# Optimization experiments

Measured on AMD Instinct MI355X. Metric: run time of the kernel, lower is better.

Reference implementation:

```python
import jax, jax.numpy as jnp
import numpy as np

N = 50000      # nodes
E = 800000     # edges (avg degree 16)
IN, H, OUT = 512, 128, 64
L = 4          # num GCN layers
ALPHA = 0.1


def setup_inputs() -> dict:
    key = jax.random.key(0)
    ks = jax.random.split(key, 9)
    # GPRGNN layer weights: temp[k] = alpha*(1-alpha)^k, temp[L] = (1-alpha)^L
    temp = ALPHA * (1.0 - ALPHA) ** np.arange(L + 1)
    temp[-1] = (1.0 - ALPHA) ** L
    return {
        "x": jax.random.normal(ks[0], (N, IN), jnp.float32),
        "w": jax.random.uniform(ks[1], (E,), jnp.float32),
        "W_in": jax.random.normal(ks[2], (IN, H), jnp.float32) * (1.0 / np.sqrt(IN)),
        "b_in": jnp.zeros((H,), jnp.float32),
        "Wl": jax.random.normal(ks[3], (L, H, H), jnp.float32) * (1.0 / np.sqrt(H)),
        "bl": jnp.zeros((L, H), jnp.float32),
        "temp": jnp.asarray(temp, jnp.float32),
        "W_out": jax.random.normal(ks[4], (H, OUT), jnp.float32) * (1.0 / np.sqrt(H)),
        "b_out": jnp.zeros((OUT,), jnp.float32),
        "src": jax.random.randint(ks[5], (E,), 0, N, jnp.int32),
        "dst": jax.random.randint(ks[6], (E,), 0, N, jnp.int32),
    }


def reference(x, w, W_in, b_in, Wl, bl, temp, W_out, b_out, src, dst):
    # input linear projection
    h = x @ W_in + b_in                         # [N, H]
    hidden = temp[0] * h
    xcur = h
    for i in range(L):
        m = xcur @ Wl[i] + bl[i]                # per-layer GCN linear, [N, H]
        msg = w[:, None] * m[src]               # weighted gather, [E, H]
        agg = jax.ops.segment_sum(msg, dst, num_segments=N)  # scatter-sum, [N, H]
        xcur = jax.nn.relu(agg)                 # (dropout is eval-mode no-op)
        hidden = hidden + temp[i + 1] * xcur
    return hidden @ W_out + b_out               # [N, OUT]
```

## Files before the change

### kernel.cpp

```cpp
#include <hip/hip_runtime.h>


typedef __attribute__((ext_vector_type(8))) short short8;
typedef __attribute__((ext_vector_type(4))) float f32x4;

__device__ __forceinline__ unsigned short f2bf(float f) {
  union { float f; unsigned u; } c{f};
  unsigned u = c.u;
  return (unsigned short)((u + 0x7fff + ((u >> 16) & 1)) >> 16);
}
__device__ __forceinline__ float bf2f_lo(unsigned v) {
  return __uint_as_float(v << 16);
}
__device__ __forceinline__ float bf2f_hi(unsigned v) {
  return __uint_as_float(v & 0xffff0000u);
}
__device__ __forceinline__ unsigned pack2bf(float a, float b) {
  return (unsigned)f2bf(a) | ((unsigned)f2bf(b) << 16);
}

__device__ __forceinline__ void gll16(const void* g, void* l) {
  __builtin_amdgcn_global_load_lds(
      (const __attribute__((address_space(1))) unsigned int*)g,
      (__attribute__((address_space(3))) unsigned int*)l, 16, 0, 0);
}

__global__ void hist_kernel(const int* __restrict__ dst, int* __restrict__ deg, int E) {
  int e = blockIdx.x * blockDim.x + threadIdx.x;
  if (e < E) atomicAdd(&deg[dst[e]], 1);
}

__global__ __launch_bounds__(256) void scan_partial(const int* __restrict__ deg,
                                                    int* __restrict__ bsum, int N) {
  int b = blockIdx.x, t = threadIdx.x;
  int lane = t & 63, wave = t >> 6;
  int i0 = b * 1024 + t * 4;
  int s = 0;
  if (i0 + 3 < N) {
    int4 v = *(const int4*)&deg[i0];
    s = v.x + v.y + v.z + v.w;
  } else {
    for (int k = 0; k < 4; ++k)
      if (i0 + k < N) s += deg[i0 + k];
  }
  for (int d = 32; d; d >>= 1) s += __shfl_down(s, d, 64);
  __shared__ int ws[4];
  if (lane == 0) ws[wave] = s;
  __syncthreads();
  if (t == 0) bsum[b] = ws[0] + ws[1] + ws[2] + ws[3];
}

__global__ void scan_base(const int* __restrict__ bsum, int* __restrict__ base, int nb) {
  int l = threadIdx.x;
  int v = (l < nb) ? bsum[l] : 0;
  int incl = v;
  for (int d = 1; d < 64; d <<= 1) {
    int t = __shfl_up(incl, d, 64);
    if (l >= d) incl += t;
  }
  if (l < nb) base[l] = incl - v;
}

__global__ __launch_bounds__(256) void scan_emit(const int* __restrict__ deg,
                                                 const int* __restrict__ base,
                                                 int* __restrict__ rowptr,
                                                 int* __restrict__ cursor, int N, int E) {
  int b = blockIdx.x, t = threadIdx.x;
  int lane = t & 63, wave = t >> 6;
  int i0 = b * 1024 + t * 4;
  int d0 = 0, d1 = 0, d2 = 0, d3 = 0;
  if (i0 + 3 < N) {
    int4 v = *(const int4*)&deg[i0];
    d0 = v.x; d1 = v.y; d2 = v.z; d3 = v.w;
  } else {
    if (i0 < N) d0 = deg[i0];
    if (i0 + 1 < N) d1 = deg[i0 + 1];
    if (i0 + 2 < N) d2 = deg[i0 + 2];
    if (i0 + 3 < N) d3 = deg[i0 + 3];
  }
  int s = d0 + d1 + d2 + d3;
  int incl = s;
  for (int d = 1; d < 64; d <<= 1) {
    int tv = __shfl_up(incl, d, 64);
    if (lane >= d) incl += tv;
  }
  __shared__ int ws[4];
  if (lane == 63) ws[wave] = incl;
  __syncthreads();
  int woff = 0;
  for (int wv = 0; wv < wave; ++wv) woff += ws[wv];
  int off = base[b] + woff + incl - s;
  if (i0 < N)     { rowptr[i0] = off;                cursor[i0] = off; }
  if (i0 + 1 < N) { int o = off + d0;                rowptr[i0+1] = o; cursor[i0+1] = o; }
  if (i0 + 2 < N) { int o = off + d0 + d1;           rowptr[i0+2] = o; cursor[i0+2] = o; }
  if (i0 + 3 < N) { int o = off + d0 + d1 + d2;      rowptr[i0+3] = o; cursor[i0+3] = o; }
  if (b == 0 && t == 0) rowptr[N] = E;
}

__global__ void fill_kernel(const int* __restrict__ src, const int* __restrict__ dst,
                            const float* __restrict__ w, int* __restrict__ cursor,
                            int* __restrict__ esrc, float* __restrict__ ew, int E) {
  int e = blockIdx.x * blockDim.x + threadIdx.x;
  if (e < E) {
    int d = dst[e];
    int p = atomicAdd(&cursor[d], 1);
    esrc[p] = src[e];
    ew[p] = w[e];
  }
}

__global__ void conv_w_kernel(const float* __restrict__ W_in,
                              const float* __restrict__ Wl,
                              unsigned short* __restrict__ WinT,
                              unsigned short* __restrict__ WlT) {
  int o = blockIdx.x * blockDim.x + threadIdx.x;
  if (o < 65536) {
    int n = o >> 9, k = o & 511;
    WinT[o] = f2bf(W_in[k * 128 + n]);
  } else if (o < 131072) {
    int p = o - 65536;
    int layer = p >> 14, n = (p >> 7) & 127, k = p & 127;
    WlT[p] = f2bf(Wl[layer * 16384 + k * 128 + n]);
  }
}

template <int K, bool CONV, bool INMODE>
__global__ __launch_bounds__(256) void gemm_bf16(
    const void* __restrict__ Ain, const unsigned short* __restrict__ BT,
    const float* __restrict__ bias, unsigned short* __restrict__ Cb,
    float* __restrict__ hidden, const float* __restrict__ temp, int M) {
  __shared__ unsigned short As[128 * 32];
  __shared__ unsigned short Bs[128 * 32];

  const int tid = threadIdx.x;
  const int lane = tid & 63;
  const int wave = tid >> 6;
  const int wm = (wave & 1) * 64;
  const int wn = (wave >> 1) * 64;
  const int blockRow = blockIdx.x * 128;

  f32x4 acc[4][4];
#pragma unroll
  for (int i = 0; i < 4; ++i)
#pragma unroll
    for (int j = 0; j < 4; ++j) acc[i][j] = (f32x4){0.f, 0.f, 0.f, 0.f};

  for (int k0 = 0; k0 < K; k0 += 32) {
    __syncthreads();
    if (CONV) {
      const float* A = (const float*)Ain;
      int row = tid >> 1;
      int kc = (tid & 1) * 16;
      int grow = blockRow + row;
      if (grow >= M) grow = M - 1;
      const float* s = &A[(size_t)grow * K + k0 + kc];
      float4 v0 = *(const float4*)(s);
      float4 v1 = *(const float4*)(s + 4);
      float4 v2 = *(const float4*)(s + 8);
      float4 v3 = *(const float4*)(s + 12);
      uint4 p0, p1;
      p0.x = pack2bf(v0.x, v0.y); p0.y = pack2bf(v0.z, v0.w);
      p0.z = pack2bf(v1.x, v1.y); p0.w = pack2bf(v1.z, v1.w);
      p1.x = pack2bf(v2.x, v2.y); p1.y = pack2bf(v2.z, v2.w);
      p1.z = pack2bf(v3.x, v3.y); p1.w = pack2bf(v3.z, v3.w);
      *(uint4*)&As[row * 32 + kc] = p0;
      *(uint4*)&As[row * 32 + kc + 8] = p1;
    } else {
      const unsigned short* A = (const unsigned short*)Ain;
#pragma unroll
      for (int ch = wave; ch < 8; ch += 4) {
        int row = ch * 16 + (lane >> 2);
        int grow = blockRow + row;
        if (grow >= M) grow = M - 1;
        gll16(&A[(size_t)grow * K + k0 + (lane & 3) * 8], (char*)As + ch * 1024);
      }
    }
#pragma unroll
    for (int ch = wave; ch < 8; ch += 4) {
      int row = ch * 16 + (lane >> 2);
      gll16(&BT[(size_t)row * K + k0 + (lane & 3) * 8], (char*)Bs + ch * 1024);
    }
    __syncthreads();

    short8 af[4], bfr[4];
#pragma unroll
    for (int i = 0; i < 4; ++i)
      af[i] = *(const short8*)&As[(wm + i * 16 + (lane & 15)) * 32 + (lane >> 4) * 8];
#pragma unroll
    for (int j = 0; j < 4; ++j)
      bfr[j] = *(const short8*)&Bs[(wn + j * 16 + (lane & 15)) * 32 + (lane >> 4) * 8];
#pragma unroll
    for (int i = 0; i < 4; ++i)
#pragma unroll
      for (int j = 0; j < 4; ++j)
        acc[i][j] =
            __builtin_amdgcn_mfma_f32_16x16x32_bf16(af[i], bfr[j], acc[i][j], 0, 0, 0);
  }

  float t0 = INMODE ? temp[0] : 0.f;
#pragma unroll
  for (int j = 0; j < 4; ++j) {
    int col = wn + j * 16 + (lane & 15);
    float bj = bias[col];
#pragma unroll
    for (int i = 0; i < 4; ++i) {
#pragma unroll
      for (int r = 0; r < 4; ++r) {
        int row = blockRow + wm + i * 16 + (lane >> 4) * 4 + r;
        if (row < M) {
          float v = acc[i][j][r] + bj;
          Cb[(size_t)row * 128 + col] = f2bf(v);
          if (INMODE) hidden[(size_t)row * 128 + col] = t0 * v;
        }
      }
    }
  }
}

__global__ __launch_bounds__(256) void agg_bf16(
    const int* __restrict__ rowptr, const int* __restrict__ esrc,
    const float* __restrict__ ew, const unsigned short* __restrict__ mb,
    unsigned short* __restrict__ xnext, float* __restrict__ hidden,
    const float* __restrict__ temp, int tempidx, int N, int write_x) {
  int node = (int)((blockIdx.x * blockDim.x + threadIdx.x) >> 6);
  int lane = threadIdx.x & 63;
  if (node >= N) return;
  const int half = lane >> 5;
  const int sl = lane & 31;
  int beg = rowptr[node];
  int end = rowptr[node + 1];

  float aA[4] = {0.f, 0.f, 0.f, 0.f}, aB[4] = {0.f, 0.f, 0.f, 0.f};
  float aC[4] = {0.f, 0.f, 0.f, 0.f}, aD[4] = {0.f, 0.f, 0.f, 0.f};

  int j = beg;
  for (; j + 8 <= end; j += 8) {
    int sA = esrc[j + half];     float wA = ew[j + half];
    int sB = esrc[j + 2 + half]; float wB = ew[j + 2 + half];
    int sC = esrc[j + 4 + half]; float wC = ew[j + 4 + half];
    int sD = esrc[j + 6 + half]; float wD = ew[j + 6 + half];
    uint2 vA = *(const uint2*)&mb[(size_t)sA * 128 + sl * 4];
    uint2 vB = *(const uint2*)&mb[(size_t)sB * 128 + sl * 4];
    uint2 vC = *(const uint2*)&mb[(size_t)sC * 128 + sl * 4];
    uint2 vD = *(const uint2*)&mb[(size_t)sD * 128 + sl * 4];
    aA[0] = fmaf(wA, bf2f_lo(vA.x), aA[0]); aA[1] = fmaf(wA, bf2f_hi(vA.x), aA[1]);
    aA[2] = fmaf(wA, bf2f_lo(vA.y), aA[2]); aA[3] = fmaf(wA, bf2f_hi(vA.y), aA[3]);
    aB[0] = fmaf(wB, bf2f_lo(vB.x), aB[0]); aB[1] = fmaf(wB, bf2f_hi(vB.x), aB[1]);
    aB[2] = fmaf(wB, bf2f_lo(vB.y), aB[2]); aB[3] = fmaf(wB, bf2f_hi(vB.y), aB[3]);
    aC[0] = fmaf(wC, bf2f_lo(vC.x), aC[0]); aC[1] = fmaf(wC, bf2f_hi(vC.x), aC[1]);
    aC[2] = fmaf(wC, bf2f_lo(vC.y), aC[2]); aC[3] = fmaf(wC, bf2f_hi(vC.y), aC[3]);
    aD[0] = fmaf(wD, bf2f_lo(vD.x), aD[0]); aD[1] = fmaf(wD, bf2f_hi(vD.x), aD[1]);
    aD[2] = fmaf(wD, bf2f_lo(vD.y), aD[2]); aD[3] = fmaf(wD, bf2f_hi(vD.y), aD[3]);
  }
  for (; j + 2 <= end; j += 2) {
    int s = esrc[j + half];
    float wt = ew[j + half];
    uint2 v = *(const uint2*)&mb[(size_t)s * 128 + sl * 4];
    aA[0] = fmaf(wt, bf2f_lo(v.x), aA[0]); aA[1] = fmaf(wt, bf2f_hi(v.x), aA[1]);
    aA[2] = fmaf(wt, bf2f_lo(v.y), aA[2]); aA[3] = fmaf(wt, bf2f_hi(v.y), aA[3]);
  }
  if (j < end) {
    int s = esrc[j];
    float wt = half ? 0.f : ew[j];
    uint2 v = *(const uint2*)&mb[(size_t)s * 128 + sl * 4];
    aA[0] = fmaf(wt, bf2f_lo(v.x), aA[0]); aA[1] = fmaf(wt, bf2f_hi(v.x), aA[1]);
    aA[2] = fmaf(wt, bf2f_lo(v.y), aA[2]); aA[3] = fmaf(wt, bf2f_hi(v.y), aA[3]);
  }

  float r[4];
#pragma unroll
  for (int k = 0; k < 4; ++k) {
    float s = (aA[k] + aB[k]) + (aC[k] + aD[k]);
    s += __shfl_xor(s, 32, 64);
    r[k] = fmaxf(s, 0.f);
  }

  if (half == 0) {
    size_t o = (size_t)node * 128 + sl * 4;
    if (write_x) {
      uint2 pk;
      pk.x = pack2bf(r[0], r[1]);
      pk.y = pack2bf(r[2], r[3]);
      *(uint2*)&xnext[o] = pk;
    }
    float tv = temp[tempidx];
    float4 h = *(const float4*)&hidden[o];
    h.x = fmaf(tv, r[0], h.x);
    h.y = fmaf(tv, r[1], h.y);
    h.z = fmaf(tv, r[2], h.z);
    h.w = fmaf(tv, r[3], h.w);
    *(float4*)&hidden[o] = h;
  }
}

__device__ __forceinline__ void fma4(float4& a, float s, const float4& w) {
  a.x = fmaf(s, w.x, a.x);
  a.y = fmaf(s, w.y, a.y);
  a.z = fmaf(s, w.z, a.z);
  a.w = fmaf(s, w.w, a.w);
}

template <int NCOL>
__global__ __launch_bounds__(256) void gemm_f32(
    const float* __restrict__ A, const float* __restrict__ W,
    const float* __restrict__ bias, float* __restrict__ C, int M, int K) {
  constexpr int KT = 64;
  constexpr int CG = NCOL / 8;
  constexpr int RG = 256 / CG;
  constexpr int MROWS = RG * 4;
  constexpr int ACH = MROWS / 4;
  constexpr int WCH = NCOL / 4;

  __shared__ float xs[MROWS * KT];
  __shared__ float wsh[KT * NCOL];

  const int tid = threadIdx.x;
  const int lane = tid & 63;
  const int wave = tid >> 6;
  const int c = tid % CG;
  const int rg = tid / CG;
  const int blockRow = blockIdx.x * MROWS;

  float4 acc0[4], acc1[4];
#pragma unroll
  for (int r = 0; r < 4; ++r) {
    acc0[r] = make_float4(0.f, 0.f, 0.f, 0.f);
    acc1[r] = make_float4(0.f, 0.f, 0.f, 0.f);
  }

  for (int k0 = 0; k0 < K; k0 += KT) {
    __syncthreads();
    for (int ch = wave; ch < ACH; ch += 4) {
      int b = ch * 1024 + lane * 16;
      int row = b >> 8;
      int kb = b & 255;
      int grow = blockRow + row;
      if (grow >= M) grow = M - 1;
      gll16(&A[(size_t)grow * K + k0 + (kb >> 2)], (char*)xs + (size_t)ch * 1024);
    }
    for (int ch = wave; ch < WCH; ch += 4) {
      int b = ch * 1024 + lane * 16;
      int kr = b / (NCOL * 4);
      int cb = b % (NCOL * 4);
      gll16(&W[(size_t)(k0 + kr) * NCOL + (cb >> 2)], (char*)wsh + (size_t)ch * 1024);
    }
    __syncthreads();

#pragma unroll
    for (int k = 0; k < KT; k += 4) {
      float4 av[4];
#pragma unroll
      for (int r = 0; r < 4; ++r)
        av[r] = *reinterpret_cast<const float4*>(&xs[(rg * 4 + r) * KT + k]);
      float4 w0[4], w1[4];
#pragma unroll
      for (int kk = 0; kk < 4; ++kk) {
        w0[kk] = *reinterpret_cast<const float4*>(&wsh[(k + kk) * NCOL + c * 4]);
        w1[kk] = *reinterpret_cast<const float4*>(&wsh[(k + kk) * NCOL + NCOL / 2 + c * 4]);
      }
#pragma unroll
      for (int r = 0; r < 4; ++r) {
        fma4(acc0[r], av[r].x, w0[0]);
        fma4(acc0[r], av[r].y, w0[1]);
        fma4(acc0[r], av[r].z, w0[2]);
        fma4(acc0[r], av[r].w, w0[3]);
        fma4(acc1[r], av[r].x, w1[0]);
        fma4(acc1[r], av[r].y, w1[1]);
        fma4(acc1[r], av[r].z, w1[2]);
        fma4(acc1[r], av[r].w, w1[3]);
      }
    }
  }

  float4 b0 = *reinterpret_cast<const float4*>(&bias[c * 4]);
  float4 b1 = *reinterpret_cast<const float4*>(&bias[NCOL / 2 + c * 4]);
#pragma unroll
  for (int r = 0; r < 4; ++r) {
    int row = blockRow + rg * 4 + r;
    if (row >= M) continue;
    float4 v0 = acc0[r], v1 = acc1[r];
    v0.x += b0.x; v0.y += b0.y; v0.z += b0.z; v0.w += b0.w;
    v1.x += b1.x; v1.y += b1.y; v1.z += b1.z; v1.w += b1.w;
    *reinterpret_cast<float4*>(&C[(size_t)row * NCOL + c * 4]) = v0;
    *reinterpret_cast<float4*>(&C[(size_t)row * NCOL + NCOL / 2 + c * 4]) = v1;
  }
}

extern "C" void kernel_launch(void* const* d_in, const int* in_sizes, int n_in,
                              void* d_out, int out_size, void* d_ws, size_t ws_size,
                              hipStream_t stream) {
  const float* x     = (const float*)d_in[0];
  const float* w     = (const float*)d_in[1];
  const float* W_in  = (const float*)d_in[2];
  const float* b_in  = (const float*)d_in[3];
  const float* Wl    = (const float*)d_in[4];
  const float* bl    = (const float*)d_in[5];
  const float* temp  = (const float*)d_in[6];
  const float* W_out = (const float*)d_in[7];
  const float* b_out = (const float*)d_in[8];
  const int*   src   = (const int*)d_in[9];
  const int*   dst   = (const int*)d_in[10];

  const int IN = 512, H = 128, L = 4;
  const int N = in_sizes[0] / IN;
  const int E = in_sizes[1];
  const int NB = (N + 1023) / 1024;

  char* p = (char*)d_ws;
  auto alloc = [&](size_t bytes) {
    void* r = (void*)p;
    p += (bytes + 255) & ~(size_t)255;
    return r;
  };
  unsigned short* xcur_b = (unsigned short*)alloc((size_t)N * H * 2);
  unsigned short* mbuf_b = (unsigned short*)alloc((size_t)N * H * 2);
  float* hidden          = (float*)alloc((size_t)N * H * sizeof(float));
  unsigned short* WinT   = (unsigned short*)alloc((size_t)H * IN * 2);
  unsigned short* WlT    = (unsigned short*)alloc((size_t)L * H * H * 2);
  int*   deg    = (int*)alloc((size_t)N * sizeof(int));
  int*   rowptr = (int*)alloc((size_t)(N + 1) * sizeof(int));
  int*   cursor = (int*)alloc((size_t)N * sizeof(int));
  int*   esrc   = (int*)alloc((size_t)E * sizeof(int));
  float* ew     = (float*)alloc((size_t)E * sizeof(float));
  int*   bsum   = (int*)alloc(64 * sizeof(int));
  int*   base   = (int*)alloc(64 * sizeof(int));

  hipMemsetAsync(deg, 0, (size_t)N * sizeof(int), stream);
  hist_kernel<<<(E + 255) / 256, 256, 0, stream>>>(dst, deg, E);
  scan_partial<<<NB, 256, 0, stream>>>(deg, bsum, N);
  scan_base<<<1, 64, 0, stream>>>(bsum, base, NB);
  scan_emit<<<NB, 256, 0, stream>>>(deg, base, rowptr, cursor, N, E);
  fill_kernel<<<(E + 255) / 256, 256, 0, stream>>>(src, dst, w, cursor, esrc, ew, E);
  conv_w_kernel<<<512, 256, 0, stream>>>(W_in, Wl, WinT, WlT);

  const int gB = (N + 127) / 128;

  gemm_bf16<512, true, true><<<gB, 256, 0, stream>>>(x, WinT, b_in, xcur_b, hidden,
                                                     temp, N);

  for (int i = 0; i < L; ++i) {
    gemm_bf16<128, false, false><<<gB, 256, 0, stream>>>(
        xcur_b, WlT + (size_t)i * H * H, bl + (size_t)i * H, mbuf_b, nullptr, temp, N);
    agg_bf16<<<(N + 3) / 4, 256, 0, stream>>>(rowptr, esrc, ew, mbuf_b, xcur_b, hidden,
                                              temp, i + 1, N, (i < L - 1) ? 1 : 0);
  }

  gemm_f32<64><<<(N + 127) / 128, 256, 0, stream>>>(hidden, W_out, b_out,
                                                    (float*)d_out, N, H);
}
```

Baseline: 524.7 us.

## Split aggregation feature dimension into four column-quarter blocks per node

The aggregation kernel now launches four times as many blocks. Each wave handles one node and one 32-column quarter of the 128-wide feature row, and each lane loads a single bf16 value per edge instead of four. This raises parallelism and memory-level concurrency in the gather. In exchange, rowptr, esrc and ew are reread four times per node, global loads shrink to 2-byte per lane (64-byte segments per half-wave), and the stores to hidden and xnext become scalar.

Result: slower. 771.9 us (+47.1%).

```diff
diff --git a/kernel.cpp b/kernel.cpp
--- a/kernel.cpp
+++ b/kernel.cpp
@@ -9,11 +9,8 @@
   unsigned u = c.u;
   return (unsigned short)((u + 0x7fff + ((u >> 16) & 1)) >> 16);
 }
-__device__ __forceinline__ float bf2f_lo(unsigned v) {
-  return __uint_as_float(v << 16);
-}
-__device__ __forceinline__ float bf2f_hi(unsigned v) {
-  return __uint_as_float(v & 0xffff0000u);
+__device__ __forceinline__ float bf2f(unsigned short v) {
+  return __uint_as_float((unsigned)v << 16);
 }
 __device__ __forceinline__ unsigned pack2bf(float a, float b) {
   return (unsigned)f2bf(a) | ((unsigned)f2bf(b) << 16);
@@ -217,79 +214,61 @@
   }
 }
 
-__global__ __launch_bounds__(256) void agg_bf16(
+__global__ __launch_bounds__(256) void agg_q(
     const int* __restrict__ rowptr, const int* __restrict__ esrc,
     const float* __restrict__ ew, const unsigned short* __restrict__ mb,
     unsigned short* __restrict__ xnext, float* __restrict__ hidden,
-    const float* __restrict__ temp, int tempidx, int N, int write_x) {
-  int node = (int)((blockIdx.x * blockDim.x + threadIdx.x) >> 6);
-  int lane = threadIdx.x & 63;
+    const float* __restrict__ temp, int tempidx, int N, int write_x,
+    int nodeBlocks) {
+  const int bid = blockIdx.x;
+  const int q = bid / nodeBlocks;
+  const int nb = bid - q * nodeBlocks;
+  const int wave = threadIdx.x >> 6;
+  const int lane = threadIdx.x & 63;
+  const int node = nb * 4 + wave;
   if (node >= N) return;
   const int half = lane >> 5;
   const int sl = lane & 31;
+  const unsigned short* mq = mb + q * 32 + sl;
+
   int beg = rowptr[node];
   int end = rowptr[node + 1];
 
-  float aA[4] = {0.f, 0.f, 0.f, 0.f}, aB[4] = {0.f, 0.f, 0.f, 0.f};
-  float aC[4] = {0.f, 0.f, 0.f, 0.f}, aD[4] = {0.f, 0.f, 0.f, 0.f};
-
+  float a0 = 0.f, a1 = 0.f, a2 = 0.f, a3 = 0.f;
   int j = beg;
   for (; j + 8 <= end; j += 8) {
     int sA = esrc[j + half];     float wA = ew[j + half];
     int sB = esrc[j + 2 + half]; float wB = ew[j + 2 + half];
     int sC = esrc[j + 4 + half]; float wC = ew[j + 4 + half];
     int sD = esrc[j + 6 + half]; float wD = ew[j + 6 + half];
-    uint2 vA = *(const uint2*)&mb[(size_t)sA * 128 + sl * 4];
-    uint2 vB = *(const uint2*)&mb[(size_t)sB * 128 + sl * 4];
-    uint2 vC = *(const uint2*)&mb[(size_t)sC * 128 + sl * 4];
-    uint2 vD = *(const uint2*)&mb[(size_t)sD * 128 + sl * 4];
-    aA[0] = fmaf(wA, bf2f_lo(vA.x), aA[0]); aA[1] = fmaf(wA, bf2f_hi(vA.x), aA[1]);
-    aA[2] = fmaf(wA, bf2f_lo(vA.y), aA[2]); aA[3] = fmaf(wA, bf2f_hi(vA.y), aA[3]);
-    aB[0] = fmaf(wB, bf2f_lo(vB.x), aB[0]); aB[1] = fmaf(wB, bf2f_hi(vB.x), aB[1]);
-    aB[2] = fmaf(wB, bf2f_lo(vB.y), aB[2]); aB[3] = fmaf(wB, bf2f_hi(vB.y), aB[3]);
-    aC[0] = fmaf(wC, bf2f_lo(vC.x), aC[0]); aC[1] = fmaf(wC, bf2f_hi(vC.x), aC[1]);
-    aC[2] = fmaf(wC, bf2f_lo(vC.y), aC[2]); aC[3] = fmaf(wC, bf2f_hi(vC.y), aC[3]);
-    aD[0] = fmaf(wD, bf2f_lo(vD.x), aD[0]); aD[1] = fmaf(wD, bf2f_hi(vD.x), aD[1]);
-    aD[2] = fmaf(wD, bf2f_lo(vD.y), aD[2]); aD[3] = fmaf(wD, bf2f_hi(vD.y), aD[3]);
+    float vA = bf2f(mq[(size_t)sA * 128]);
+    float vB = bf2f(mq[(size_t)sB * 128]);
+    float vC = bf2f(mq[(size_t)sC * 128]);
+    float vD = bf2f(mq[(size_t)sD * 128]);
+    a0 = fmaf(wA, vA, a0);
+    a1 = fmaf(wB, vB, a1);
+    a2 = fmaf(wC, vC, a2);
+    a3 = fmaf(wD, vD, a3);
   }
   for (; j + 2 <= end; j += 2) {
     int s = esrc[j + half];
     float wt = ew[j + half];
-    uint2 v = *(const uint2*)&mb[(size_t)s * 128 + sl * 4];
-    aA[0] = fmaf(wt, bf2f_lo(v.x), aA[0]); aA[1] = fmaf(wt, bf2f_hi(v.x), aA[1]);
-    aA[2] = fmaf(wt, bf2f_lo(v.y), aA[2]); aA[3] = fmaf(wt, bf2f_hi(v.y), aA[3]);
+    a0 = fmaf(wt, bf2f(mq[(size_t)s * 128]), a0);
   }
   if (j < end) {
     int s = esrc[j];
     float wt = half ? 0.f : ew[j];
-    uint2 v = *(const uint2*)&mb[(size_t)s * 128 + sl * 4];
-    aA[0] = fmaf(wt, bf2f_lo(v.x), aA[0]); aA[1] = fmaf(wt, bf2f_hi(v.x), aA[1]);
-    aA[2] = fmaf(wt, bf2f_lo(v.y), aA[2]); aA[3] = fmaf(wt, bf2f_hi(v.y), aA[3]);
-  }
-
-  float r[4];
-#pragma unroll
-  for (int k = 0; k < 4; ++k) {
-    float s = (aA[k] + aB[k]) + (aC[k] + aD[k]);
-    s += __shfl_xor(s, 32, 64);
-    r[k] = fmaxf(s, 0.f);
-  }
+    a0 = fmaf(wt, bf2f(mq[(size_t)s * 128]), a0);
+  }
+
+  float s = (a0 + a1) + (a2 + a3);
+  s += __shfl_xor(s, 32, 64);
 
   if (half == 0) {
-    size_t o = (size_t)node * 128 + sl * 4;
-    if (write_x) {
-      uint2 pk;
-      pk.x = pack2bf(r[0], r[1]);
-      pk.y = pack2bf(r[2], r[3]);
-      *(uint2*)&xnext[o] = pk;
-    }
-    float tv = temp[tempidx];
-    float4 h = *(const float4*)&hidden[o];
-    h.x = fmaf(tv, r[0], h.x);
-    h.y = fmaf(tv, r[1], h.y);
-    h.z = fmaf(tv, r[2], h.z);
-    h.w = fmaf(tv, r[3], h.w);
-    *(float4*)&hidden[o] = h;
+    float r = fmaxf(s, 0.f);
+    size_t o = (size_t)node * 128 + q * 32 + sl;
+    if (write_x) xnext[o] = f2bf(r);
+    hidden[o] = fmaf(temp[tempidx], r, hidden[o]);
   }
 }
 
@@ -434,6 +413,7 @@
   conv_w_kernel<<<512, 256, 0, stream>>>(W_in, Wl, WinT, WlT);
 
   const int gB = (N + 127) / 128;
+  const int nodeBlocks = (N + 3) / 4;
 
   gemm_bf16<512, true, true><<<gB, 256, 0, stream>>>(x, WinT, b_in, xcur_b, hidden,
                                                      temp, N);
@@ -441,8 +421,9 @@
   for (int i = 0; i < L; ++i) {
     gemm_bf16<128, false, false><<<gB, 256, 0, stream>>>(
         xcur_b, WlT + (size_t)i * H * H, bl + (size_t)i * H, mbuf_b, nullptr, temp, N);
-    agg_bf16<<<(N + 3) / 4, 256, 0, stream>>>(rowptr, esrc, ew, mbuf_b, xcur_b, hidden,
-                                              temp, i + 1, N, (i < L - 1) ? 1 : 0);
+    agg_q<<<4 * nodeBlocks, 256, 0, stream>>>(rowptr, esrc, ew, mbuf_b, xcur_b, hidden,
+                                              temp, i + 1, N, (i < L - 1) ? 1 : 0,
+                                              nodeBlocks);
   }
 
   gemm_f32<64><<<(N + 127) / 128, 256, 0, stream>>>(hidden, W_out, b_out,
```

## Store all layer outputs in bf16 and fuse hidden sum into MFMA output GEMM

Applied to the files above, without the earlier changes.

Removes the fp32 hidden accumulator, which each aggregation pass read and wrote. Each layer's bf16 output is now kept in its own buffer. A new output kernel forms the temp-weighted sum of all five buffers, rounds it to bf16 in LDS, and applies W_out with bf16 MFMA instead of an fp32 scalar GEMM. The aggregation kernel now has each lane load 16-byte rows with four edge groups per wave, which needs one more shuffle reduction. This cuts fp32 read-modify-write traffic but needs more workspace and loses some precision from bf16 rounding of the hidden sum.

Result: faster. 506.7 us (-3.4%).

```diff
diff --git a/kernel.cpp b/kernel.cpp
--- a/kernel.cpp
+++ b/kernel.cpp
@@ -111,8 +111,10 @@
 
 __global__ void conv_w_kernel(const float* __restrict__ W_in,
                               const float* __restrict__ Wl,
+                              const float* __restrict__ W_out,
                               unsigned short* __restrict__ WinT,
-                              unsigned short* __restrict__ WlT) {
+                              unsigned short* __restrict__ WlT,
+                              unsigned short* __restrict__ WoutT) {
   int o = blockIdx.x * blockDim.x + threadIdx.x;
   if (o < 65536) {
     int n = o >> 9, k = o & 511;
@@ -121,14 +123,17 @@
     int p = o - 65536;
     int layer = p >> 14, n = (p >> 7) & 127, k = p & 127;
     WlT[p] = f2bf(Wl[layer * 16384 + k * 128 + n]);
-  }
-}
-
-template <int K, bool CONV, bool INMODE>
+  } else if (o < 139264) {
+    int p = o - 131072;
+    int n = p >> 7, k = p & 127;
+    WoutT[p] = f2bf(W_out[k * 64 + n]);
+  }
+}
+
+template <int K, bool CONV>
 __global__ __launch_bounds__(256) void gemm_bf16(
     const void* __restrict__ Ain, const unsigned short* __restrict__ BT,
-    const float* __restrict__ bias, unsigned short* __restrict__ Cb,
-    float* __restrict__ hidden, const float* __restrict__ temp, int M) {
+    const float* __restrict__ bias, unsigned short* __restrict__ Cb, int M) {
   __shared__ unsigned short As[128 * 32];
   __shared__ unsigned short Bs[128 * 32];
 
@@ -197,7 +202,6 @@
             __builtin_amdgcn_mfma_f32_16x16x32_bf16(af[i], bfr[j], acc[i][j], 0, 0, 0);
   }
 
-  float t0 = INMODE ? temp[0] : 0.f;
 #pragma unroll
   for (int j = 0; j < 4; ++j) {
     int col = wn + j * 16 + (lane & 15);
@@ -207,182 +211,169 @@
 #pragma unroll
       for (int r = 0; r < 4; ++r) {
         int row = blockRow + wm + i * 16 + (lane >> 4) * 4 + r;
-        if (row < M) {
-          float v = acc[i][j][r] + bj;
-          Cb[(size_t)row * 128 + col] = f2bf(v);
-          if (INMODE) hidden[(size_t)row * 128 + col] = t0 * v;
-        }
+        if (row < M) Cb[(size_t)row * 128 + col] = f2bf(acc[i][j][r] + bj);
       }
     }
   }
 }
 
-__global__ __launch_bounds__(256) void agg_bf16(
+__global__ __launch_bounds__(256) void agg_v3(
     const int* __restrict__ rowptr, const int* __restrict__ esrc,
     const float* __restrict__ ew, const unsigned short* __restrict__ mb,
-    unsigned short* __restrict__ xnext, float* __restrict__ hidden,
-    const float* __restrict__ temp, int tempidx, int N, int write_x) {
-  int node = (int)((blockIdx.x * blockDim.x + threadIdx.x) >> 6);
-  int lane = threadIdx.x & 63;
+    unsigned short* __restrict__ xnext, int N) {
+  const int node = blockIdx.x * 4 + (threadIdx.x >> 6);
+  const int lane = threadIdx.x & 63;
   if (node >= N) return;
-  const int half = lane >> 5;
-  const int sl = lane & 31;
-  int beg = rowptr[node];
-  int end = rowptr[node + 1];
-
-  float aA[4] = {0.f, 0.f, 0.f, 0.f}, aB[4] = {0.f, 0.f, 0.f, 0.f};
-  float aC[4] = {0.f, 0.f, 0.f, 0.f}, aD[4] = {0.f, 0.f, 0.f, 0.f};
+  const int g = lane >> 4;
+  const int c = lane & 15;
+  const int beg = rowptr[node];
+  const int end = rowptr[node + 1];
+  const unsigned short* mc = mb + c * 8;
+
+  float aA[8] = {0.f, 0.f, 0.f, 0.f, 0.f, 0.f, 0.f, 0.f};
+  float aB[8] = {0.f, 0.f, 0.f, 0.f, 0.f, 0.f, 0.f, 0.f};
 
   int j = beg;
   for (; j + 8 <= end; j += 8) {
-    int sA = esrc[j + half];     float wA = ew[j + half];
-    int sB = esrc[j + 2 + half]; float wB = ew[j + 2 + half];
-    int sC = esrc[j + 4 + half]; float wC = ew[j + 4 + half];
-    int sD = esrc[j + 6 + half]; float wD = ew[j + 6 + half];
-    uint2 vA = *(const uint2*)&mb[(size_t)sA * 128 + sl * 4];
-    uint2 vB = *(const uint2*)&mb[(size_t)sB * 128 + sl * 4];
-    uint2 vC = *(const uint2*)&mb[(size_t)sC * 128 + sl * 4];
-    uint2 vD = *(const uint2*)&mb[(size_t)sD * 128 + sl * 4];
+    int sA = esrc[j + g];     float wA = ew[j + g];
+    int sB = esrc[j + 4 + g]; float wB = ew[j + 4 + g];
+    uint4 vA = *(const uint4*)&mc[(size_t)sA * 128];
+    uint4 vB = *(const uint4*)&mc[(size_t)sB * 128];
     aA[0] = fmaf(wA, bf2f_lo(vA.x), aA[0]); aA[1] = fmaf(wA, bf2f_hi(vA.x), aA[1]);
     aA[2] = fmaf(wA, bf2f_lo(vA.y), aA[2]); aA[3] = fmaf(wA, bf2f_hi(vA.y), aA[3]);
+    aA[4] = fmaf(wA, bf2f_lo(vA.z), aA[4]); aA[5] = fmaf(wA, bf2f_hi(vA.z), aA[5]);
+    aA[6] = fmaf(wA, bf2f_lo(vA.w), aA[6]); aA[7] = fmaf(wA, bf2f_hi(vA.w), aA[7]);
     aB[0] = fmaf(wB, bf2f_lo(vB.x), aB[0]); aB[1] = fmaf(wB, bf2f_hi(vB.x), aB[1]);
     aB[2] = fmaf(wB, bf2f_lo(vB.y), aB[2]); aB[3] = fmaf(wB, bf2f_hi(vB.y), aB[3]);
-    aC[0] = fmaf(wC, bf2f_lo(vC.x), aC[0]); aC[1] = fmaf(wC, bf2f_hi(vC.x), aC[1]);
-    aC[2] = fmaf(wC, bf2f_lo(vC.y), aC[2]); aC[3] = fmaf(wC, bf2f_hi(vC.y), aC[3]);
-    aD[0] = fmaf(wD, bf2f_lo(vD.x), aD[0]); aD[1] = fmaf(wD, bf2f_hi(vD.x), aD[1]);
-    aD[2] = fmaf(wD, bf2f_lo(vD.y), aD[2]); aD[3] = fmaf(wD, bf2f_hi(vD.y), aD[3]);
-  }
-  for (; j + 2 <= end; j += 2) {
-    int s = esrc[j + half];
-    float wt = ew[j + half];
-    uint2 v = *(const uint2*)&mb[(size_t)s * 128 + sl * 4];
+    aB[4] = fmaf(wB, bf2f_lo(vB.z), aB[4]); aB[5] = fmaf(wB, bf2f_hi(vB.z), aB[5]);
+    aB[6] = fmaf(wB, bf2f_lo(vB.w), aB[6]); aB[7] = fmaf(wB, bf2f_hi(vB.w), aB[7]);
+  }
+  if (j + 4 <= end) {
+    int s = esrc[j + g]; float wt = ew[j + g];
+    uint4 v = *(const uint4*)&mc[(size_t)s * 128];
     aA[0] = fmaf(wt, bf2f_lo(v.x), aA[0]); aA[1] = fmaf(wt, bf2f_hi(v.x), aA[1]);
     aA[2] = fmaf(wt, bf2f_lo(v.y), aA[2]); aA[3] = fmaf(wt, bf2f_hi(v.y), aA[3]);
+    aA[4] = fmaf(wt, bf2f_lo(v.z), aA[4]); aA[5] = fmaf(wt, bf2f_hi(v.z), aA[5]);
+    aA[6] = fmaf(wt, bf2f_lo(v.w), aA[6]); aA[7] = fmaf(wt, bf2f_hi(v.w), aA[7]);
+    j += 4;
   }
   if (j < end) {
-    int s = esrc[j];
-    float wt = half ? 0.f : ew[j];
-    uint2 v = *(const uint2*)&mb[(size_t)s * 128 + sl * 4];
-    aA[0] = fmaf(wt, bf2f_lo(v.x), aA[0]); aA[1] = fmaf(wt, bf2f_hi(v.x), aA[1]);
-    aA[2] = fmaf(wt, bf2f_lo(v.y), aA[2]); aA[3] = fmaf(wt, bf2f_hi(v.y), aA[3]);
-  }
-
-  float r[4];
-#pragma unroll
-  for (int k = 0; k < 4; ++k) {
-    float s = (aA[k] + aB[k]) + (aC[k] + aD[k]);
+    int idx = j + g;
+    int s = esrc[(idx < end) ? idx : (end - 1)];
+    float wt = (idx < end) ? ew[idx] : 0.f;
+    uint4 v = *(const uint4*)&mc[(size_t)s * 128];
+    aB[0] = fmaf(wt, bf2f_lo(v.x), aB[0]); aB[1] = fmaf(wt, bf2f_hi(v.x), aB[1]);
+    aB[2] = fmaf(wt, bf2f_lo(v.y), aB[2]); aB[3] = fmaf(wt, bf2f_hi(v.y), aB[3]);
+    aB[4] = fmaf(wt, bf2f_lo(v.z), aB[4]); aB[5] = fmaf(wt, bf2f_hi(v.z), aB[5]);
+    aB[6] = fmaf(wt, bf2f_lo(v.w), aB[6]); aB[7] = fmaf(wt, bf2f_hi(v.w), aB[7]);
+  }
+
+  float r[8];
+#pragma unroll
+  for (int k = 0; k < 8; ++k) {
+    float s = aA[k] + aB[k];
+    s += __shfl_xor(s, 16, 64);
     s += __shfl_xor(s, 32, 64);
     r[k] = fmaxf(s, 0.f);
   }
-
-  if (half == 0) {
-    size_t o = (size_t)node * 128 + sl * 4;
-    if (write_x) {
-      uint2 pk;
-      pk.x = pack2bf(r[0], r[1]);
-      pk.y = pack2bf(r[2], r[3]);
-      *(uint2*)&xnext[o] = pk;
-    }
-    float tv = temp[tempidx];
-    float4 h = *(const float4*)&hidden[o];
-    h.x = fmaf(tv, r[0], h.x);
-    h.y = fmaf(tv, r[1], h.y);
-    h.z = fmaf(tv, r[2], h.z);
-    h.w = fmaf(tv, r[3], h.w);
-    *(float4*)&hidden[o] = h;
-  }
-}
-
-__device__ __forceinline__ void fma4(float4& a, float s, const float4& w) {
-  a.x = fmaf(s, w.x, a.x);
-  a.y = fmaf(s, w.y, a.y);
-  a.z = fmaf(s, w.z, a.z);
-  a.w = fmaf(s, w.w, a.w);
-}
-
-template <int NCOL>
-__global__ __launch_bounds__(256) void gemm_f32(
-    const float* __restrict__ A, const float* __restrict__ W,
-    const float* __restrict__ bias, float* __restrict__ C, int M, int K) {
-  constexpr int KT = 64;
-  constexpr int CG = NCOL / 8;
-  constexpr int RG = 256 / CG;
-  constexpr int MROWS = RG * 4;
-  constexpr int ACH = MROWS / 4;
-  constexpr int WCH = NCOL / 4;
-
-  __shared__ float xs[MROWS * KT];
-  __shared__ float wsh[KT * NCOL];
+  if (g == 0) {
+    uint4 pk;
+    pk.x = pack2bf(r[0], r[1]);
+    pk.y = pack2bf(r[2], r[3]);
+    pk.z = pack2bf(r[4], r[5]);
+    pk.w = pack2bf(r[6], r[7]);
+    *(uint4*)&xnext[(size_t)node * 128 + c * 8] = pk;
+  }
+}
+
+__global__ __launch_bounds__(256) void gemm_out(
+    const unsigned short* __restrict__ xb,
+    const float* __restrict__ temp, const unsigned short* __restrict__ WoT,
+    const float* __restrict__ b_out, float* __restrict__ out, int M) {
+  __shared__ unsigned short As[128 * 136];
+  __shared__ unsigned short Bs[64 * 136];
 
   const int tid = threadIdx.x;
   const int lane = tid & 63;
   const int wave = tid >> 6;
-  const int c = tid % CG;
-  const int rg = tid / CG;
-  const int blockRow = blockIdx.x * MROWS;
-
-  float4 acc0[4], acc1[4];
-#pragma unroll
-  for (int r = 0; r < 4; ++r) {
-    acc0[r] = make_float4(0.f, 0.f, 0.f, 0.f);
-    acc1[r] = make_float4(0.f, 0.f, 0.f, 0.f);
-  }
-
-  for (int k0 = 0; k0 < K; k0 += KT) {
-    __syncthreads();
-    for (int ch = wave; ch < ACH; ch += 4) {
-      int b = ch * 1024 + lane * 16;
-      int row = b >> 8;
-      int kb = b & 255;
-      int grow = blockRow + row;
-      if (grow >= M) grow = M - 1;
-      gll16(&A[(size_t)grow * K + k0 + (kb >> 2)], (char*)xs + (size_t)ch * 1024);
+  const int blockRow = blockIdx.x * 128;
+
+  float t[5];
+#pragma unroll
+  for (int i = 0; i < 5; ++i) t[i] = temp[i];
+
+  {
+    int row = tid >> 1;
+    int grow = blockRow + row;
+    if (grow >= M) grow = M - 1;
+    int ch0 = (tid & 1) * 64;
+#pragma unroll
+    for (int gch = 0; gch < 64; gch += 8) {
+      float acc[8] = {0.f, 0.f, 0.f, 0.f, 0.f, 0.f, 0.f, 0.f};
+#pragma unroll
+      for (int i = 0; i < 5; ++i) {
+        uint4 v = *(const uint4*)&xb[((size_t)i * M + grow) * 128 + ch0 + gch];
+        acc[0] = fmaf(t[i], bf2f_lo(v.x), acc[0]);
+        acc[1] = fmaf(t[i], bf2f_hi(v.x), acc[1]);
+        acc[2] = fmaf(t[i], bf2f_lo(v.y), acc[2]);
+        acc[3] = fmaf(t[i], bf2f_hi(v.y), acc[3]);
+        acc[4] = fmaf(t[i], bf2f_lo(v.z), acc[4]);
+        acc[5] = fmaf(t[i], bf2f_hi(v.z), acc[5]);
+        acc[6] = fmaf(t[i], bf2f_lo(v.w), acc[6]);
+        acc[7] = fmaf(t[i], bf2f_hi(v.w), acc[7]);
+      }
+      uint4 pk;
+      pk.x = pack2bf(acc[0], acc[1]);
+      pk.y = pack2bf(acc[2], acc[3]);
+      pk.z = pack2bf(acc[4], acc[5]);
+      pk.w = pack2bf(acc[6], acc[7]);
+      *(uint4*)&As[row * 136 + ch0 + gch] = pk;
     }
-    for (int ch = wave; ch < WCH; ch += 4) {
-      int b = ch * 1024 + lane * 16;
-      int kr = b / (NCOL * 4);
-      int cb = b % (NCOL * 4);
-      gll16(&W[(size_t)(k0 + kr) * NCOL + (cb >> 2)], (char*)wsh + (size_t)ch * 1024);
-    }
-    __syncthreads();
-
-#pragma unroll
-    for (int k = 0; k < KT; k += 4) {
-      float4 av[4];
-#pragma unroll
-      for (int r = 0; r < 4; ++r)
-        av[r] = *reinterpret_cast<const float4*>(&xs[(rg * 4 + r) * KT + k]);
-      float4 w0[4], w1[4];
-#pragma unroll
-      for (int kk = 0; kk < 4; ++kk) {
-        w0[kk] = *reinterpret_cast<const float4*>(&wsh[(k + kk) * NCOL + c * 4]);
-        w1[kk] = *reinterpret_cast<const float4*>(&wsh[(k + kk) * NCOL + NCOL / 2 + c * 4]);
-      }
+  }
+  for (int i = tid; i < 64 * 16; i += 256) {
+    int row = i >> 4;
+    int chunk = (i & 15) * 8;
+    *(uint4*)&Bs[row * 136 + chunk] = *(const uint4*)&WoT[row * 128 + chunk];
+  }
+  __syncthreads();
+
+  f32x4 acc[2][4];
+#pragma unroll
+  for (int i = 0; i < 2; ++i)
+#pragma unroll
+    for (int j = 0; j < 4; ++j) acc[i][j] = (f32x4){0.f, 0.f, 0.f, 0.f};
+
+#pragma unroll
+  for (int kf = 0; kf < 4; ++kf) {
+    short8 af[2], bfr[4];
+#pragma unroll
+    for (int i = 0; i < 2; ++i)
+      af[i] = *(const short8*)&As[(wave * 32 + i * 16 + (lane & 15)) * 136 + kf * 32 +
+                                  (lane >> 4) * 8];
+#pragma unroll
+    for (int j = 0; j < 4; ++j)
+      bfr[j] = *(const short8*)&Bs[(j * 16 + (lane & 15)) * 136 + kf * 32 +
+                                   (lane >> 4) * 8];
+#pragma unroll
+    for (int i = 0; i < 2; ++i)
+#pragma unroll
+      for (int j = 0; j < 4; ++j)
+        acc[i][j] =
+            __builtin_amdgcn_mfma_f32_16x16x32_bf16(af[i], bfr[j], acc[i][j], 0, 0, 0);
+  }
+
+#pragma unroll
+  for (int j = 0; j < 4; ++j) {
+    int col = j * 16 + (lane & 15);
+    float bj = b_out[col];
+#pragma unroll
+    for (int i = 0; i < 2; ++i) {
 #pragma unroll
       for (int r = 0; r < 4; ++r) {
-        fma4(acc0[r], av[r].x, w0[0]);
-        fma4(acc0[r], av[r].y, w0[1]);
-        fma4(acc0[r], av[r].z, w0[2]);
-        fma4(acc0[r], av[r].w, w0[3]);
-        fma4(acc1[r], av[r].x, w1[0]);
-        fma4(acc1[r], av[r].y, w1[1]);
-        fma4(acc1[r], av[r].z, w1[2]);
-        fma4(acc1[r], av[r].w, w1[3]);
+        int row = blockRow + wave * 32 + i * 16 + (lane >> 4) * 4 + r;
+        if (row < M) out[(size_t)row * 64 + col] = acc[i][j][r] + bj;
       }
     }
-  }
-
-  float4 b0 = *reinterpret_cast<const float4*>(&bias[c * 4]);
-  float4 b1 = *reinterpret_cast<const float4*>(&bias[NCOL / 2 + c * 4]);
-#pragma unroll
-  for (int r = 0; r < 4; ++r) {
-    int row = blockRow + rg * 4 + r;
-    if (row >= M) continue;
-    float4 v0 = acc0[r], v1 = acc1[r];
-    v0.x += b0.x; v0.y += b0.y; v0.z += b0.z; v0.w += b0.w;
-    v1.x += b1.x; v1.y += b1.y; v1.z += b1.z; v1.w += b1.w;
-    *reinterpret_cast<float4*>(&C[(size_t)row * NCOL + c * 4]) = v0;
-    *reinterpret_cast<float4*>(&C[(size_t)row * NCOL + NCOL / 2 + c * 4]) = v1;
   }
 }
 
@@ -405,6 +396,7 @@
   const int N = in_sizes[0] / IN;
   const int E = in_sizes[1];
   const int NB = (N + 1023) / 1024;
+  const size_t NH = (size_t)N * H;
 
   char* p = (char*)d_ws;
   auto alloc = [&](size_t bytes) {
@@ -412,11 +404,11 @@
     p += (bytes + 255) & ~(size_t)255;
     return r;
   };
-  unsigned short* xcur_b = (unsigned short*)alloc((size_t)N * H * 2);
-  unsigned short* mbuf_b = (unsigned short*)alloc((size_t)N * H * 2);
-  float* hidden          = (float*)alloc((size_t)N * H * sizeof(float));
+  unsigned short* xb     = (unsigned short*)alloc(5 * NH * 2);
+  unsigned short* mbuf_b = (unsigned short*)alloc(NH * 2);
   unsigned short* WinT   = (unsigned short*)alloc((size_t)H * IN * 2);
   unsigned short* WlT    = (unsigned short*)alloc((size_t)L * H * H * 2);
+  unsigned short* WoutT  = (unsigned short*)alloc((size_t)64 * H * 2);
   int*   deg    = (int*)alloc((size_t)N * sizeof(int));
   int*   rowptr = (int*)alloc((size_t)(N + 1) * sizeof(int));
   int*   cursor = (int*)alloc((size_t)N * sizeof(int));
@@ -431,20 +423,18 @@
   scan_base<<<1, 64, 0, stream>>>(bsum, base, NB);
   scan_emit<<<NB, 256, 0, stream>>>(deg, base, rowptr, cursor, N, E);
   fill_kernel<<<(E + 255) / 256, 256, 0, stream>>>(src, dst, w, cursor, esrc, ew, E);
-  conv_w_kernel<<<512, 256, 0, stream>>>(W_in, Wl, WinT, WlT);
+  conv_w_kernel<<<544, 256, 0, stream>>>(W_in, Wl, W_out, WinT, WlT, WoutT);
 
   const int gB = (N + 127) / 128;
 
-  gemm_bf16<512, true, true><<<gB, 256, 0, stream>>>(x, WinT, b_in, xcur_b, hidden,
-                                                     temp, N);
+  gemm_bf16<512, true><<<gB, 256, 0, stream>>>(x, WinT, b_in, xb, N);
 
   for (int i = 0; i < L; ++i) {
-    gemm_bf16<128, false, false><<<gB, 256, 0, stream>>>(
-        xcur_b, WlT + (size_t)i * H * H, bl + (size_t)i * H, mbuf_b, nullptr, temp, N);
-    agg_bf16<<<(N + 3) / 4, 256, 0, stream>>>(rowptr, esrc, ew, mbuf_b, xcur_b, hidden,
-                                              temp, i + 1, N, (i < L - 1) ? 1 : 0);
-  }
-
-  gemm_f32<64><<<(N + 127) / 128, 256, 0, stream>>>(hidden, W_out, b_out,
-                                                    (float*)d_out, N, H);
-}
+    gemm_bf16<128, false><<<gB, 256, 0, stream>>>(
+        xb + (size_t)i * NH, WlT + (size_t)i * H * H, bl + (size_t)i * H, mbuf_b, N);
+    agg_v3<<<(N + 3) / 4, 256, 0, stream>>>(rowptr, esrc, ew, mbuf_b,
+                                            xb + (size_t)(i + 1) * NH, N);
+  }
+
+  gemm_out<<<gB, 256, 0, stream>>>(xb, temp, WoutT, b_out, (float*)d_out, N);
+}
```
